# Performance work log

Measured on AMD Instinct MI355X. Metric: run time of the kernel, lower is better.

Reference implementation:

```python
import jax, jax.numpy as jnp
import numpy as np

WS = 7          # window size
NH = 8          # num heads
EPS = 1e-5


def _rel_pos_index(ws):
    # timm WindowAttention relative_position_index, shape (ws*ws, ws*ws), values in [0, (2ws-1)^2)
    coords = np.stack(np.meshgrid(np.arange(ws), np.arange(ws), indexing='ij'))  # 2,ws,ws
    coords = coords.reshape(2, -1)
    rel = coords[:, :, None] - coords[:, None, :]          # 2,N,N
    rel = rel.transpose(1, 2, 0)                           # N,N,2
    rel[:, :, 0] += ws - 1
    rel[:, :, 1] += ws - 1
    rel[:, :, 0] *= 2 * ws - 1
    return rel.sum(-1)                                     # N,N

RPI = jnp.asarray(_rel_pos_index(WS), dtype=jnp.int32)


def _ln(x, g, b):
    mu = jnp.mean(x, axis=-1, keepdims=True)
    var = jnp.mean(jnp.square(x - mu), axis=-1, keepdims=True)
    return (x - mu) * jax.lax.rsqrt(var + EPS) * g + b


def setup_inputs() -> dict:
    key = jax.random.key(0)
    ks = jax.random.split(key, 16)
    C, Hd, V = 256, 1024, 7
    s = lambda k, shp, fan: jax.random.normal(k, shp, jnp.float32) * (fan ** -0.5)
    return {
        'x': jax.random.normal(ks[0], (256, 256, 14, 14), jnp.float32),
        'conv_w': s(ks[1], (C, C), C), 'conv_b': jnp.zeros((C,), jnp.float32),
        'ln1_g': jnp.ones((C,), jnp.float32), 'ln1_b': jnp.zeros((C,), jnp.float32),
        'qkv_w': s(ks[2], (C, 3 * C), C), 'qkv_b': jnp.zeros((3 * C,), jnp.float32),
        'rpb': 0.02 * jax.random.normal(ks[3], ((2 * WS - 1) ** 2, NH), jnp.float32),
        'proj_w': s(ks[4], (C, C), C), 'proj_b': jnp.zeros((C,), jnp.float32),
        'ln2_g': jnp.ones((C,), jnp.float32), 'ln2_b': jnp.zeros((C,), jnp.float32),
        'fc1_w': s(ks[5], (C, Hd), C), 'fc1_b': jnp.zeros((Hd,), jnp.float32),
        'fc2_w': s(ks[6], (Hd, C), Hd), 'fc2_b': jnp.zeros((C,), jnp.float32),
        'fc_out_w': s(ks[7], (C, V), C), 'fc_out_b': jnp.zeros((V,), jnp.float32),
    }


def reference(x, conv_w, conv_b, ln1_g, ln1_b, qkv_w, qkv_b, rpb, proj_w, proj_b,
              ln2_g, ln2_b, fc1_w, fc1_b, fc2_w, fc2_b, fc_out_w, fc_out_b):
    B, Cin, H, W = x.shape
    C = conv_w.shape[0]
    hd = C // NH
    # 1x1 conv projection -> tokens (B, H*W, C)
    t = jnp.einsum('oc,bchw->bhwo', conv_w, x) + conv_b            # B,H,W,C
    tok = t.reshape(B, H * W, C)
    # --- Swin block, shift_size=0 ---
    shortcut = tok
    y = _ln(tok, ln1_g, ln1_b).reshape(B, H, W, C)
    # window partition -> (B*nW, ws*ws, C)
    nHw, nWw = H // WS, W // WS
    yw = y.reshape(B, nHw, WS, nWw, WS, C).transpose(0, 1, 3, 2, 4, 5)
    yw = yw.reshape(B * nHw * nWw, WS * WS, C)
    N = WS * WS
    qkv = (yw @ qkv_w + qkv_b).reshape(-1, N, 3, NH, hd).transpose(2, 0, 3, 1, 4)
    q, k, v = qkv[0], qkv[1], qkv[2]                               # (Bn, NH, N, hd)
    attn = jnp.einsum('bhqd,bhkd->bhqk', q * (hd ** -0.5), k)
    attn = attn + rpb[RPI].transpose(2, 0, 1)[None]                # + (NH,N,N) bias
    attn = jax.nn.softmax(attn, axis=-1)
    o = jnp.einsum('bhqk,bhkd->bqhd', attn, v).reshape(-1, N, C)
    o = o @ proj_w + proj_b
    # window reverse
    o = o.reshape(B, nHw, nWw, WS, WS, C).transpose(0, 1, 3, 2, 4, 5).reshape(B, H * W, C)
    tok = shortcut + o                                             # drop_path = identity (eval)
    h = _ln(tok, ln2_g, ln2_b)
    h = jax.nn.gelu(h @ fc1_w + fc1_b, approximate=False) @ fc2_w + fc2_b
    tok = tok + h
    # global average pool over spatial tokens, then classifier
    pooled = jnp.mean(tok, axis=1)                                 # B,C
    return pooled @ fc_out_w + fc_out_b
```

## Files before the change

kernel.cpp:

```cpp
#include <hip/hip_runtime.h>
#include <math.h>

#define NHEADS 8
#define BATCH  256
#define HWTOK  196
#define MTOT   50176

#define BM 128
#define BN 128
#define BK 64

typedef short bfrag8 __attribute__((ext_vector_type(8)));
typedef float ffrag4 __attribute__((ext_vector_type(4)));

__device__ __forceinline__ unsigned short f2bf(float f) {
  union { float f; unsigned u; } v; v.f = f;
  unsigned r = v.u + 0x7fffu + ((v.u >> 16) & 1u);
  return (unsigned short)(r >> 16);
}
__device__ __forceinline__ float bf2f(unsigned short b) {
  union { unsigned u; float f; } v; v.u = ((unsigned)b) << 16;
  return v.f;
}
__device__ __forceinline__ float gelu_exact(float x) {
  return 0.5f * x * (1.0f + erff(x * 0.70710678118654752f));
}
__device__ __forceinline__ int window_reverse_row(int m) {
  int widx = m / 49, pos = m % 49;
  int b = widx >> 2, wh = (widx >> 1) & 1, ww = widx & 1;
  int i = pos / 7, j = pos % 7;
  return b * 196 + (wh * 7 + i) * 14 + (ww * 7 + j);
}

__device__ __forceinline__ void gload16(const void* g, void* l) {
  __builtin_amdgcn_global_load_lds(
      (const __attribute__((address_space(1))) void*)g,
      (__attribute__((address_space(3))) void*)l, 16, 0, 0);
}

template <int EPI>
__global__ __launch_bounds__(256) void k_gemm_mfma(const unsigned short* __restrict__ A,
                                                   const unsigned short* __restrict__ BT,
                                                   const float* __restrict__ bias,
                                                   void* __restrict__ Cout,
                                                   int rowbase, int N, int K, int nMt) {
  __shared__ __align__(128) unsigned short S[32768];
  const int t = threadIdx.x;
  const int lane = t & 63, w = t >> 6;
  const int wr = w >> 1, wc = w & 1;
  const int m_t = blockIdx.x % nMt, n_t = blockIdx.x / nMt;
  const int m0 = m_t * BM, n0 = n_t * BN;
  const int l15 = lane & 15;
  const int sw = (lane & 7) << 3;
  const int rA = lane >> 3;
  const int kin = (((lane & 7) ^ rA) << 3);
  ffrag4 acc[4][4] = {};

#define STAGE(buf, k0_)                                                         \
  {                                                                             \
    _Pragma("unroll")                                                           \
    for (int i = 0; i < 4; ++i) {                                               \
      const int seg = i * 4 + w;                                                \
      const int row = seg * 8 + rA;                                             \
      gload16(A + (size_t)(m0 + row) * K + (k0_) + kin,                         \
              (char*)S + (buf) * 16384 + seg * 1024);                           \
      gload16(BT + (size_t)(n0 + row) * K + (k0_) + kin,                        \
              (char*)S + 32768 + (buf) * 16384 + seg * 1024);                   \
    }                                                                           \
  }

  STAGE(0, 0);
  __syncthreads();
  int cur = 0;
  for (int k0 = 0; k0 < K; k0 += BK) {
    if (k0 + BK < K) STAGE(cur ^ 1, k0 + BK);
    const int ab = cur * 8192, bb = 16384 + cur * 8192;
#pragma unroll
    for (int kk = 0; kk < BK; kk += 32) {
      bfrag8 af[4], bfr[4];
      const int colA = (kk + (lane >> 4) * 8) ^ sw;
#pragma unroll
      for (int mi = 0; mi < 4; ++mi) {
        int row = wr * 64 + mi * 16 + l15;
        af[mi] = *(const bfrag8*)&S[ab + row * BK + colA];
      }
#pragma unroll
      for (int ni = 0; ni < 4; ++ni) {
        int col = wc * 64 + ni * 16 + l15;
        bfr[ni] = *(const bfrag8*)&S[bb + col * BK + colA];
      }
#pragma unroll
      for (int mi = 0; mi < 4; ++mi)
#pragma unroll
        for (int ni = 0; ni < 4; ++ni)
          acc[mi][ni] = __builtin_amdgcn_mfma_f32_16x16x32_bf16(af[mi], bfr[ni], acc[mi][ni], 0, 0, 0);
    }
    __syncthreads();
    cur ^= 1;
  }
#undef STAGE

  const int cr = (lane >> 4) * 4;
  const int cc = l15;
  float bv[4];
#pragma unroll
  for (int ni = 0; ni < 4; ++ni) bv[ni] = bias[n0 + wc * 64 + ni * 16 + cc];

  if (EPI == 0 || EPI == 1) {
#pragma unroll
    for (int mi = 0; mi < 4; ++mi) {
#pragma unroll
      for (int j = 0; j < 4; ++j) {
        const int ml = wr * 64 + mi * 16 + cr + j;
#pragma unroll
        for (int ni = 0; ni < 4; ++ni) {
          const int nl = wc * 64 + ni * 16 + cc;
          float v = acc[mi][ni][j] + bv[ni];
          if (EPI == 1) v = gelu_exact(v);
          S[ml * 128 + nl] = f2bf(v);
        }
      }
    }
    __syncthreads();
#pragma unroll
    for (int r = 0; r < 8; ++r) {
      const int flat = (r * 256 + t) * 8;
      const int ml = flat >> 7, nl = flat & 127;
      uint4 vv = *(const uint4*)&S[flat];
      *(uint4*)((unsigned short*)Cout + (size_t)(m0 + ml) * N + n0 + nl) = vv;
    }
  } else {
#pragma unroll
    for (int mi = 0; mi < 4; ++mi) {
#pragma unroll
      for (int j = 0; j < 4; ++j) {
        const int m = m0 + wr * 64 + mi * 16 + cr + j;
        int row;
        if (EPI == 2) row = window_reverse_row(rowbase + m);
        else if (EPI == 3) row = rowbase + m;
        else row = m;
#pragma unroll
        for (int ni = 0; ni < 4; ++ni) {
          const int n = n0 + wc * 64 + ni * 16 + cc;
          float v = acc[mi][ni][j] + bv[ni];
          if (EPI == 4) {
            ((float*)Cout)[(size_t)row * N + n] = v;
          } else {
            float* p = (float*)Cout + (size_t)row * N + n;
            *p += v;
          }
        }
      }
    }
  }
}

__global__ __launch_bounds__(256) void k_wtrans(const float* __restrict__ w,
                                                unsigned short* __restrict__ wt,
                                                int K, int N) {
  __shared__ float tile[32][33];
  int k0 = blockIdx.x * 32, n0 = blockIdx.y * 32;
  int tx = threadIdx.x & 31, ty = threadIdx.x >> 5;
#pragma unroll
  for (int r = 0; r < 4; ++r)
    tile[ty + r * 8][tx] = w[(size_t)(k0 + ty + r * 8) * N + n0 + tx];
  __syncthreads();
#pragma unroll
  for (int r = 0; r < 4; ++r)
    wt[(size_t)(n0 + ty + r * 8) * K + k0 + tx] = f2bf(tile[tx][ty + r * 8]);
}

__global__ __launch_bounds__(256) void k_cast(const float* __restrict__ w,
                                              unsigned short* __restrict__ wb, int n) {
  int i = blockIdx.x * 256 + threadIdx.x;
  if (i < n) wb[i] = f2bf(w[i]);
}

__global__ __launch_bounds__(256) void k_transpose_x(const float* __restrict__ x,
                                                     unsigned short* __restrict__ xt) {
  __shared__ float tile[32][33];
  int b = blockIdx.x;
  int hw0 = blockIdx.y * 32;
  int c0 = blockIdx.z * 32;
  int tx = threadIdx.x & 31, ty = threadIdx.x >> 5;
#pragma unroll
  for (int r = 0; r < 4; ++r) {
    int c = c0 + ty + r * 8, hw = hw0 + tx;
    if (hw < HWTOK) tile[ty + r * 8][tx] = x[((size_t)b * 256 + c) * HWTOK + hw];
  }
  __syncthreads();
#pragma unroll
  for (int r = 0; r < 4; ++r) {
    int hw = hw0 + ty + r * 8, c = c0 + tx;
    if (hw < HWTOK) xt[((size_t)b * HWTOK + hw) * 256 + c] = f2bf(tile[tx][ty + r * 8]);
  }
}

template <bool WINDOW>
__global__ __launch_bounds__(256) void k_layernorm(const float* __restrict__ in,
                                                   const float* __restrict__ g,
                                                   const float* __restrict__ bta,
                                                   unsigned short* __restrict__ out,
                                                   int rowbase) {
  int wid = threadIdx.x >> 6, lane = threadIdx.x & 63;
  int li = blockIdx.x * 4 + wid;
  int token = rowbase + li;
  const float4 xv = *(const float4*)(in + (size_t)token * 256 + lane * 4);
  float s = xv.x + xv.y + xv.z + xv.w;
  float sq = xv.x * xv.x + xv.y * xv.y + xv.z * xv.z + xv.w * xv.w;
#pragma unroll
  for (int off = 32; off >= 1; off >>= 1) {
    s += __shfl_xor(s, off);
    sq += __shfl_xor(sq, off);
  }
  float mean = s * (1.f / 256.f);
  float var = sq * (1.f / 256.f) - mean * mean;
  float rstd = rsqrtf(var + 1e-5f);
  float4 gv = *(const float4*)(g + lane * 4);
  float4 bv = *(const float4*)(bta + lane * 4);
  ushort4 ov;
  ov.x = f2bf((xv.x - mean) * rstd * gv.x + bv.x);
  ov.y = f2bf((xv.y - mean) * rstd * gv.y + bv.y);
  ov.z = f2bf((xv.z - mean) * rstd * gv.z + bv.z);
  ov.w = f2bf((xv.w - mean) * rstd * gv.w + bv.w);
  int orow;
  if (WINDOW) {
    int b = token / 196, hw = token % 196;
    int h14 = hw / 14, w14 = hw % 14;
    int wh = h14 / 7, i = h14 % 7, ww = w14 / 7, j = w14 % 7;
    int widx = (b * 2 + wh) * 2 + ww;
    orow = widx * 49 + i * 7 + j - rowbase;
  } else {
    orow = li;
  }
  *(ushort4*)(out + (size_t)orow * 256 + lane * 4) = ov;
}

__global__ __launch_bounds__(256) void k_attention(const unsigned short* __restrict__ qkv,
                                                   const float* __restrict__ rpb,
                                                   unsigned short* __restrict__ o) {
  __shared__ unsigned short Kl[4][64 * 40];
  __shared__ unsigned short VTl[4][32 * 72];
  __shared__ unsigned short Pl[4][64 * 72];
  __shared__ float rpbl[4][176];

  const int t = threadIdx.x;
  const int w4 = t >> 6, lane = t & 63;
  const int l15 = lane & 15, g = lane >> 4;
  const int gw = blockIdx.x * 4 + w4;
  const int lw = gw >> 3, head = gw & 7;

  unsigned short* K_ = Kl[w4];
  unsigned short* VT_ = VTl[w4];
  unsigned short* P_ = Pl[w4];
  float* rpb_ = rpbl[w4];

  const size_t baseq = (size_t)lw * 49 * 768 + head * 32;

  for (int e = lane; e < 169; e += 64) rpb_[e] = rpb[e * 8 + head];

  for (int e = lane; e < 512; e += 64) {
    int d = e >> 4, tk = 48 + (e & 15);
    if ((e & 15) != 0) VT_[d * 72 + tk] = 0;
  }

  for (int e = lane; e < 784; e += 64) {
    int tok = e >> 4, dp = e & 15;
    unsigned kv = *(const unsigned*)(qkv + baseq + 256 + (size_t)tok * 768 + dp * 2);
    *(unsigned*)&K_[tok * 40 + dp * 2] = kv;
    unsigned vv = *(const unsigned*)(qkv + baseq + 512 + (size_t)tok * 768 + dp * 2);
    VT_[(dp * 2 + 0) * 72 + tok] = (unsigned short)(vv & 0xffffu);
    VT_[(dp * 2 + 1) * 72 + tok] = (unsigned short)(vv >> 16);
  }

  ffrag4 acc[4][4] = {};
  {
    bfrag8 af[4], bfr[4];
#pragma unroll
    for (int qi = 0; qi < 4; ++qi)
      af[qi] = *(const bfrag8*)(qkv + baseq + (size_t)(16 * qi + l15) * 768 + g * 8);
#pragma unroll
    for (int kj = 0; kj < 4; ++kj)
      bfr[kj] = *(const bfrag8*)&K_[(16 * kj + l15) * 40 + g * 8];
#pragma unroll
    for (int qi = 0; qi < 4; ++qi)
#pragma unroll
      for (int kj = 0; kj < 4; ++kj)
        acc[qi][kj] = __builtin_amdgcn_mfma_f32_16x16x32_bf16(af[qi], bfr[kj], acc[qi][kj], 0, 0, 0);
  }

  const float scale = 0.17677669529663687f;
  int kc[4];
  bool kvalid[4];
#pragma unroll
  for (int kj = 0; kj < 4; ++kj) {
    int c = 16 * kj + l15;
    kc[kj] = 13 * (c / 7) + (c % 7);
    kvalid[kj] = (c < 49);
  }
#pragma unroll
  for (int qi = 0; qi < 4; ++qi) {
#pragma unroll
    for (int j = 0; j < 4; ++j) {
      int q = 16 * qi + 4 * g + j;
      int qc = 13 * (q / 7) + (q % 7);
      float tv[4];
#pragma unroll
      for (int kj = 0; kj < 4; ++kj)
        tv[kj] = kvalid[kj] ? (acc[qi][kj][j] * scale + rpb_[qc - kc[kj] + 84]) : -INFINITY;
      float mx = fmaxf(fmaxf(tv[0], tv[1]), fmaxf(tv[2], tv[3]));
#pragma unroll
      for (int off = 8; off >= 1; off >>= 1) mx = fmaxf(mx, __shfl_xor(mx, off));
      float p[4], sum = 0.f;
#pragma unroll
      for (int kj = 0; kj < 4; ++kj) {
        p[kj] = kvalid[kj] ? __expf(tv[kj] - mx) : 0.f;
        sum += p[kj];
      }
#pragma unroll
      for (int off = 8; off >= 1; off >>= 1) sum += __shfl_xor(sum, off);
      float inv = 1.0f / sum;
      if (q < 49) {
#pragma unroll
        for (int kj = 0; kj < 4; ++kj)
          P_[q * 72 + 16 * kj + l15] = f2bf(p[kj] * inv);
      }
    }
  }

  ffrag4 accO[2][4] = {};
#pragma unroll
  for (int kk = 0; kk < 64; kk += 32) {
    bfrag8 af2[2], bf2[4];
#pragma unroll
    for (int ti = 0; ti < 2; ++ti)
      af2[ti] = *(const bfrag8*)&VT_[(16 * ti + l15) * 72 + kk + g * 8];
#pragma unroll
    for (int qj = 0; qj < 4; ++qj)
      bf2[qj] = *(const bfrag8*)&P_[(16 * qj + l15) * 72 + kk + g * 8];
#pragma unroll
    for (int ti = 0; ti < 2; ++ti)
#pragma unroll
      for (int qj = 0; qj < 4; ++qj)
        accO[ti][qj] = __builtin_amdgcn_mfma_f32_16x16x32_bf16(af2[ti], bf2[qj], accO[ti][qj], 0, 0, 0);
  }

#pragma unroll
  for (int qj = 0; qj < 4; ++qj) {
    int q = 16 * qj + l15;
    if (q < 49) {
#pragma unroll
      for (int ti = 0; ti < 2; ++ti) {
        ushort4 ov;
        ov.x = f2bf(accO[ti][qj][0]);
        ov.y = f2bf(accO[ti][qj][1]);
        ov.z = f2bf(accO[ti][qj][2]);
        ov.w = f2bf(accO[ti][qj][3]);
        *(ushort4*)(o + ((size_t)lw * 49 + q) * 256 + head * 32 + 16 * ti + 4 * g) = ov;
      }
    }
  }
}

__global__ __launch_bounds__(256) void k_pool(const float* __restrict__ tok,
                                              float* __restrict__ pooled) {
  int b = blockIdx.x, c = threadIdx.x;
  float s = 0.f;
  for (int hw = 0; hw < 196; ++hw) s += tok[((size_t)b * 196 + hw) * 256 + c];
  pooled[b * 256 + c] = s * (1.f / 196.f);
}

__global__ __launch_bounds__(64) void k_head(const float* __restrict__ pooled,
                                             const float* __restrict__ w,
                                             const float* __restrict__ bias,
                                             float* __restrict__ out) {
  int b = blockIdx.x, t = threadIdx.x;
  if (t < 7) {
    float s = bias[t];
    for (int c = 0; c < 256; ++c) s = fmaf(pooled[b * 256 + c], w[c * 7 + t], s);
    out[b * 7 + t] = s;
  }
}

extern "C" void kernel_launch(void* const* d_in, const int* in_sizes, int n_in,
                              void* d_out, int out_size, void* d_ws, size_t ws_size,
                              hipStream_t stream) {
  const float* x      = (const float*)d_in[0];
  const float* conv_w = (const float*)d_in[1];
  const float* conv_b = (const float*)d_in[2];
  const float* ln1_g  = (const float*)d_in[3];
  const float* ln1_b  = (const float*)d_in[4];
  const float* qkv_w  = (const float*)d_in[5];
  const float* qkv_b  = (const float*)d_in[6];
  const float* rpb    = (const float*)d_in[7];
  const float* proj_w = (const float*)d_in[8];
  const float* proj_b = (const float*)d_in[9];
  const float* ln2_g  = (const float*)d_in[10];
  const float* ln2_b  = (const float*)d_in[11];
  const float* fc1_w  = (const float*)d_in[12];
  const float* fc1_b  = (const float*)d_in[13];
  const float* fc2_w  = (const float*)d_in[14];
  const float* fc2_b  = (const float*)d_in[15];
  const float* fco_w  = (const float*)d_in[16];
  const float* fco_b  = (const float*)d_in[17];
  float* out = (float*)d_out;
  char* p = (char*)d_ws;

  const size_t FULL_NEED = 207486976ull;
  const int nch = (ws_size >= FULL_NEED) ? 1 : 4;
  const int chw = 1024 / nch;
  const size_t chrows = (size_t)chw * 49;
  const int nMt = (int)(chrows / BM);

  float* tok = (float*)p;                     p += (size_t)MTOT * 256 * 4;
  unsigned short* Bbuf = (unsigned short*)p;  p += chrows * 1024 * 2;
  unsigned short* Abuf = (unsigned short*)p;  p += chrows * 256 * 2;
  unsigned short* Cbuf = (unsigned short*)p;  p += chrows * 256 * 2;
  unsigned short* cwB  = (unsigned short*)p;  p += 65536 * 2;
  unsigned short* qkvT = (unsigned short*)p;  p += 196608 * 2;
  unsigned short* projT= (unsigned short*)p;  p += 65536 * 2;
  unsigned short* fc1T = (unsigned short*)p;  p += 262144 * 2;
  unsigned short* fc2T = (unsigned short*)p;  p += 262144 * 2;
  float* pool = (float*)p;                    p += 65536 * 4;
  unsigned short* xt = Bbuf;

  k_cast<<<256, 256, 0, stream>>>(conv_w, cwB, 65536);
  k_wtrans<<<dim3(8, 24), 256, 0, stream>>>(qkv_w, qkvT, 256, 768);
  k_wtrans<<<dim3(8, 8), 256, 0, stream>>>(proj_w, projT, 256, 256);
  k_wtrans<<<dim3(8, 32), 256, 0, stream>>>(fc1_w, fc1T, 256, 1024);
  k_wtrans<<<dim3(32, 8), 256, 0, stream>>>(fc2_w, fc2T, 1024, 256);

  k_transpose_x<<<dim3(BATCH, 7, 8), 256, 0, stream>>>(x, xt);
  k_gemm_mfma<4><<<(MTOT / BM) * 2, 256, 0, stream>>>(xt, cwB, conv_b, tok, 0, 256, 256, MTOT / BM);

  for (int c = 0; c < nch; ++c) {
    const int rowbase = c * (int)chrows;
    k_layernorm<true><<<chrows / 4, 256, 0, stream>>>(tok, ln1_g, ln1_b, Abuf, rowbase);
    k_gemm_mfma<0><<<nMt * 6, 256, 0, stream>>>(Abuf, qkvT, qkv_b, Bbuf, 0, 768, 256, nMt);
    k_attention<<<chw * 2, 256, 0, stream>>>(Bbuf, rpb, Cbuf);
    k_gemm_mfma<2><<<nMt * 2, 256, 0, stream>>>(Cbuf, projT, proj_b, tok, rowbase, 256, 256, nMt);
    k_layernorm<false><<<chrows / 4, 256, 0, stream>>>(tok, ln2_g, ln2_b, Abuf, rowbase);
    k_gemm_mfma<1><<<nMt * 8, 256, 0, stream>>>(Abuf, fc1T, fc1_b, Bbuf, 0, 1024, 256, nMt);
    k_gemm_mfma<3><<<nMt * 2, 256, 0, stream>>>(Bbuf, fc2T, fc2_b, tok, rowbase, 256, 1024, nMt);
  }

  k_pool<<<BATCH, 256, 0, stream>>>(tok, pool);
  k_head<<<BATCH, 64, 0, stream>>>(pool, fco_w, fco_b, out);
}
```

Before: 371.7 us.

## Single-buffer GEMM shared memory and replace erff with polynomial GELU approximation

The GEMM kernel drops double buffering: shared memory is halved and each K step now loads a tile, synchronizes, then computes, so global loads no longer overlap with MFMA work. The smaller LDS footprint may let more blocks fit per CU. Separately, exact erf in GELU is replaced with the Abramowitz-Stegun polynomial using a fast exp, which cuts epilogue arithmetic but brings roughly 1e-7-level absolute error in erf.

```diff
diff --git a/kernel.cpp b/kernel.cpp
--- a/kernel.cpp
+++ b/kernel.cpp
@@ -23,7 +23,16 @@
   return v.f;
 }
 __device__ __forceinline__ float gelu_exact(float x) {
-  return 0.5f * x * (1.0f + erff(x * 0.70710678118654752f));
+  float ax = fabsf(x) * 0.70710678118654752f;
+  float t = 1.0f / (1.0f + 0.3275911f * ax);
+  float y = t * (0.254829592f +
+            t * (-0.284496736f +
+            t * (1.421413741f +
+            t * (-1.453152027f +
+            t * 1.061405429f))));
+  float e = 1.0f - y * __expf(-ax * ax);
+  float erfv = copysignf(e, x);
+  return 0.5f * x * (1.0f + erfv);
 }
 __device__ __forceinline__ int window_reverse_row(int m) {
   int widx = m / 49, pos = m % 49;
@@ -44,7 +53,7 @@
                                                    const float* __restrict__ bias,
                                                    void* __restrict__ Cout,
                                                    int rowbase, int N, int K, int nMt) {
-  __shared__ __align__(128) unsigned short S[32768];
+  __shared__ __align__(128) unsigned short S[16384];
   const int t = threadIdx.x;
   const int lane = t & 63, w = t >> 6;
   const int wr = w >> 1, wc = w & 1;
@@ -56,25 +65,15 @@
   const int kin = (((lane & 7) ^ rA) << 3);
   ffrag4 acc[4][4] = {};
 
-#define STAGE(buf, k0_)                                                         \
-  {                                                                             \
-    _Pragma("unroll")                                                           \
-    for (int i = 0; i < 4; ++i) {                                               \
-      const int seg = i * 4 + w;                                                \
-      const int row = seg * 8 + rA;                                             \
-      gload16(A + (size_t)(m0 + row) * K + (k0_) + kin,                         \
-              (char*)S + (buf) * 16384 + seg * 1024);                           \
-      gload16(BT + (size_t)(n0 + row) * K + (k0_) + kin,                        \
-              (char*)S + 32768 + (buf) * 16384 + seg * 1024);                   \
-    }                                                                           \
-  }
-
-  STAGE(0, 0);
-  __syncthreads();
-  int cur = 0;
   for (int k0 = 0; k0 < K; k0 += BK) {
-    if (k0 + BK < K) STAGE(cur ^ 1, k0 + BK);
-    const int ab = cur * 8192, bb = 16384 + cur * 8192;
+#pragma unroll
+    for (int i = 0; i < 4; ++i) {
+      const int seg = i * 4 + w;
+      const int row = seg * 8 + rA;
+      gload16(A + (size_t)(m0 + row) * K + k0 + kin, (char*)S + seg * 1024);
+      gload16(BT + (size_t)(n0 + row) * K + k0 + kin, (char*)S + 16384 + seg * 1024);
+    }
+    __syncthreads();
 #pragma unroll
     for (int kk = 0; kk < BK; kk += 32) {
       bfrag8 af[4], bfr[4];
@@ -82,12 +81,12 @@
 #pragma unroll
       for (int mi = 0; mi < 4; ++mi) {
         int row = wr * 64 + mi * 16 + l15;
-        af[mi] = *(const bfrag8*)&S[ab + row * BK + colA];
+        af[mi] = *(const bfrag8*)&S[row * BK + colA];
       }
 #pragma unroll
       for (int ni = 0; ni < 4; ++ni) {
         int col = wc * 64 + ni * 16 + l15;
-        bfr[ni] = *(const bfrag8*)&S[bb + col * BK + colA];
+        bfr[ni] = *(const bfrag8*)&S[8192 + col * BK + colA];
       }
 #pragma unroll
       for (int mi = 0; mi < 4; ++mi)
@@ -96,9 +95,7 @@
           acc[mi][ni] = __builtin_amdgcn_mfma_f32_16x16x32_bf16(af[mi], bfr[ni], acc[mi][ni], 0, 0, 0);
     }
     __syncthreads();
-    cur ^= 1;
-  }
-#undef STAGE
+  }
 
   const int cr = (lane >> 4) * 4;
   const int cc = l15;
```

New measurement: 356.3 us. 1.04x faster.
